# Kernel optimization log

Hardware: AMD Instinct MI355X
Metric: run time of the kernel (lower is better)

The kernel has to match this reference:

```python
import jax, jax.numpy as jnp
import numpy as np

B, S, D = 4, 2048, 512
BETA = 1.0
PARAM_SCALE = 1.0 / np.sqrt(D)  # ~ torch Linear default init scale


def setup_inputs() -> dict:
    key = jax.random.key(0)
    ks = jax.random.split(key, 14)
    def rn(k, shape, scale=1.0):
        return (jax.random.normal(k, shape, jnp.float32) * scale).astype(jnp.float32)
    return {
        "x_re": rn(ks[0], (B, S, D)),
        "x_im": rn(ks[1], (B, S, D)),
        "Wq_re": rn(ks[2], (D, D), PARAM_SCALE), "Wq_im": rn(ks[3], (D, D), PARAM_SCALE),
        "bq_re": rn(ks[4], (D,), PARAM_SCALE),   "bq_im": rn(ks[5], (D,), PARAM_SCALE),
        "Wk_re": rn(ks[6], (D, D), PARAM_SCALE), "Wk_im": rn(ks[7], (D, D), PARAM_SCALE),
        "bk_re": rn(ks[8], (D,), PARAM_SCALE),   "bk_im": rn(ks[9], (D,), PARAM_SCALE),
        "Wv_re": rn(ks[10], (D, D), PARAM_SCALE), "Wv_im": rn(ks[11], (D, D), PARAM_SCALE),
        "bv_re": rn(ks[12], (D,), PARAM_SCALE),   "bv_im": rn(ks[13], (D,), PARAM_SCALE),
    }


def reference(x_re, x_im, Wq_re, Wq_im, bq_re, bq_im,
              Wk_re, Wk_im, bk_re, bk_im, Wv_re, Wv_im, bv_re, bv_im):
    cx = lambda re, im: (re + 1j * im).astype(jnp.complex64)
    x = cx(x_re, x_im)                          # [B,S,D] complex64
    # nn.Linear: y = x @ W.T + b (complex)
    Q = jnp.einsum('bsd,ed->bse', x, cx(Wq_re, Wq_im)) + cx(bq_re, bq_im)
    K = jnp.einsum('bsd,ed->bse', x, cx(Wk_re, Wk_im)) + cx(bk_re, bk_im)
    V = jnp.einsum('bsd,ed->bse', x, cx(Wv_re, Wv_im)) + cx(bv_re, bv_im)
    # energy = -Re(Q K^H); attn = softmax(-beta * energy) = softmax(beta * Re(Q K^H))
    scores = jnp.real(jnp.einsum('bse,bte->bst', Q, jnp.conj(K)))  # [B,S,S] float32
    attn = jax.nn.softmax(BETA * scores, axis=-1)
    out = jnp.einsum('bst,bte->bse', attn.astype(jnp.complex64), V)  # [B,S,D] complex64
    return out
```

## Files before the change

kernel.cpp:

```cpp
#include <hip/hip_runtime.h>
#include <hip/hip_bf16.h>
#include <cstdint>
#include <cstddef>


typedef unsigned short u16;
typedef __attribute__((ext_vector_type(8))) _Float16 half8;
typedef __attribute__((ext_vector_type(4))) float f32x4;

#define B_    4
#define S_    2048
#define D_    512
#define M_TOT (B_ * S_)
#define KC    (2 * D_)
#define N1    (6 * D_)
#define LP    32
#define RE_PLANE 4194304

#define X_ELEMS  ((size_t)M_TOT * KC)
#define W_ELEMS  ((size_t)N1 * KC)
#define QK_ELEMS ((size_t)M_TOT * KC)
#define VT_ELEMS ((size_t)B_ * KC * S_)
#define AT_ELEMS ((size_t)M_TOT * S_)

__device__ __forceinline__ u16 f2h(float f) {
    _Float16 h = (_Float16)f;
    return __builtin_bit_cast(u16, h);
}
__device__ __forceinline__ float h2f(u16 b) {
    return (float)__builtin_bit_cast(_Float16, b);
}

__device__ __forceinline__ f32x4 mfma16(half8 a, half8 b, f32x4 c) {
    return __builtin_amdgcn_mfma_f32_16x16x32_f16(a, b, c, 0, 0, 0);
}

__device__ __forceinline__ void dma16(const u16* g, u16* l) {
    __builtin_amdgcn_global_load_lds(
        (const __attribute__((address_space(1))) unsigned int*)g,
        (__attribute__((address_space(3))) unsigned int*)l,
        16, 0, 0);
}

__device__ __forceinline__ void stage_dma(const u16* __restrict__ src, int ld,
                                          int rowbase, int kbase,
                                          u16* __restrict__ dst, int tid) {
#pragma unroll
    for (int i = 0; i < 2; ++i) {
        int c = tid + 256 * i;
        int row = c >> 2, q = c & 3;
        dma16(src + (size_t)(rowbase + row) * ld + kbase + q * 8, dst + c * 8);
    }
}

__device__ __forceinline__ void stage_half(u16* __restrict__ plane,
                                           const u16* __restrict__ src,
                                           int rowbase, int kcol, int tid) {
#pragma unroll
    for (int i = 0; i < 2; ++i) {
        int c = tid + (i << 9);
        int c2 = c ^ (((c >> 5) & 1) << 1);
        int row = ((c2 >> 3) << 1) | ((c2 >> 2) & 1);
        int ks = c2 & 3;
        dma16(src + (size_t)(rowbase + row) * KC + (kcol + ks * 8),
              plane + c * 8);
    }
}

#define VMW(N) asm volatile("s_waitcnt vmcnt(" #N ")" ::: "memory")

__global__ void k_diag(float* __restrict__ out, int out_size, float val) {
    int i = blockIdx.x * 256 + threadIdx.x;
    if (i < out_size && i < 4096) out[i] = val;
}

__global__ void k_prep(const float* __restrict__ xr, const float* __restrict__ xi,
                       const float* __restrict__ Wqr, const float* __restrict__ Wqi,
                       const float* __restrict__ Wkr, const float* __restrict__ Wki,
                       const float* __restrict__ Wvr, const float* __restrict__ Wvi,
                       const float* __restrict__ bqr, const float* __restrict__ bqi,
                       const float* __restrict__ bkr, const float* __restrict__ bki,
                       const float* __restrict__ bvr, const float* __restrict__ bvi,
                       u16* __restrict__ Xh, u16* __restrict__ Xl,
                       u16* __restrict__ Wh, float* __restrict__ bc) {
    int gb = blockIdx.x;
    int tid = threadIdx.x;
    if (gb < 16384) {
        int id = gb * 256 + tid;
        int m = id >> 9, d = id & 511;
        size_t o = (size_t)m * KC + d;
        if (o + D_ >= X_ELEMS) return;
        float vr = xr[id], vi = xi[id];
        u16 h;
        h = f2h(vr); Xh[o] = h;        Xl[o] = f2h(vr - h2f(h));
        h = f2h(vi); Xh[o + D_] = h;   Xl[o + D_] = f2h(vi - h2f(h));
    } else if (gb < 16384 + 12288) {
        int id = (gb - 16384) * 256 + tid;
        int n = id >> 10, k = id & 1023;
        int q = n >> 9, e = n & 511;
        int half = k >> 9, d = k & 511;
        const float* Wre = (q < 2) ? Wqr : ((q < 4) ? Wkr : Wvr);
        const float* Wim = (q < 2) ? Wqi : ((q < 4) ? Wki : Wvi);
        size_t src = (size_t)e * D_ + d;
        float v;
        if ((q & 1) == 0) v = half ? -Wim[src] : Wre[src];
        else              v = half ?  Wre[src] : Wim[src];
        if ((size_t)id < W_ELEMS) Wh[id] = f2h(v);
    } else {
        int id = (gb - 16384 - 12288) * 256 + tid;
        if (id >= N1) return;
        int q = id >> 9, e = id & 511;
        const float* src = (q == 0) ? bqr : (q == 1) ? bqi : (q == 2) ? bkr
                         : (q == 3) ? bki : (q == 4) ? bvr : bvi;
        bc[id] = src[e];
    }
}

#define GTILE(P, STG0, STG1, W1, STG2, STG3, W3)                              \
  {                                                                           \
    const int p_ = (P);                                                       \
    _Pragma("unroll")                                                         \
    for (int q = 0; q < 4; ++q) {                                             \
      const int kh = q >> 1, mg = q & 1;                                      \
      const u16* pa = &lds[(p_ << 2) | kh][0];                                \
      const u16* pb = &lds[(p_ << 2) | 2 | kh][0];                            \
      half8 a[4];                                                             \
      if (mg == 0) {                                                          \
        _Pragma("unroll")                                                     \
        for (int j = 0; j < 4; ++j)                                           \
          b[j] = *(const half8*)(pb + boffs + j * 512);                       \
      }                                                                       \
      _Pragma("unroll")                                                       \
      for (int i = 0; i < 4; ++i)                                             \
        a[i] = *(const half8*)(pa + aoffs + (mg * 4 + i) * 512);              \
      if (q == 0)      { STG0; }                                              \
      else if (q == 1) { STG1; W1; }                                          \
      else if (q == 2) { STG2; }                                              \
      else             { STG3; W3; }                                          \
      __builtin_amdgcn_s_barrier();                                           \
      __builtin_amdgcn_s_setprio(1);                                          \
      _Pragma("unroll")                                                       \
      for (int j = 0; j < 4; ++j) {                                           \
        _Pragma("unroll")                                                     \
        for (int i = 0; i < 4; ++i)                                           \
          acc[mg * 4 + i][j] = mfma16(a[i], b[j], acc[mg * 4 + i][j]);        \
      }                                                                       \
      __builtin_amdgcn_s_setprio(0);                                          \
      __builtin_amdgcn_s_barrier();                                           \
    }                                                                         \
  }

__global__ __launch_bounds__(512, 2) void k_gemm1(
    const u16* __restrict__ Xh, const u16* __restrict__ Xl,
    const u16* __restrict__ Wh,
    const float* __restrict__ bc,
    u16* __restrict__ Qh, u16* __restrict__ Ql,
    u16* __restrict__ Kh, u16* __restrict__ Kl,
    u16* __restrict__ VT) {
    __shared__ __attribute__((aligned(16))) u16 lds[8][8192];
    int tid = threadIdx.x;

    int orig = blockIdx.y * 12 + blockIdx.x;
    int swz = (orig & 7) * 48 + (orig >> 3);
    int bx = swz % 12, by = swz / 12;
    int nb = bx * 256, mb = by * 256;
    int g = bx >> 2;
    bool vblk = (g == 2);
    int NT = vblk ? 16 : 32;

    int lane = tid & 63, wave = tid >> 6;
    int wm = (wave >> 2) * 128, wn = (wave & 3) * 64;
    int lr = lane & 15, lq = lane >> 4;
    int lqs8 = (lq ^ (((lr >> 3) & 1) << 1)) * 8;
    int aoffs = (wm + lr) * 32 + lqs8;
    int boffs = (wn + lr) * 32 + lqs8;

    f32x4 acc[8][4] = {};
    half8 b[4];

    stage_half(&lds[0][0], Xh, mb, 0, tid);
    stage_half(&lds[2][0], Wh, nb, 0, tid);
    stage_half(&lds[1][0], Xh, mb, 32, tid);
    stage_half(&lds[3][0], Wh, nb, 32, tid);
    stage_half(&lds[4][0], Xh, mb, 64, tid);
    stage_half(&lds[6][0], Wh, nb, 64, tid);
    VMW(8);
    __builtin_amdgcn_s_barrier();

    for (int t = 0; t < NT - 2; ++t) {
        const int p = t & 1;
        const u16* s1 = (!vblk && (t + 1) >= 16) ? Xl : Xh;
        const int k1o = (((t + 1) & 15) << 6) + 32;
        const u16* s2 = (!vblk && (t + 2) >= 16) ? Xl : Xh;
        const int k2o = ((t + 2) & 15) << 6;
        GTILE(p,
              stage_half(&lds[((p ^ 1) << 2) | 1][0], s1, mb, k1o, tid),
              stage_half(&lds[((p ^ 1) << 2) | 3][0], Wh, nb, k1o, tid),
              VMW(8),
              stage_half(&lds[(p << 2) | 0][0], s2, mb, k2o, tid),
              stage_half(&lds[(p << 2) | 2][0], Wh, nb, k2o, tid),
              VMW(8));
    }
    {
        const int p = (NT - 2) & 1;
        const u16* s1 = vblk ? Xh : Xl;
        const int k1o = (((NT - 1) & 15) << 6) + 32;
        GTILE(p,
              stage_half(&lds[((p ^ 1) << 2) | 1][0], s1, mb, k1o, tid),
              stage_half(&lds[((p ^ 1) << 2) | 3][0], Wh, nb, k1o, tid),
              VMW(8),
              (void)0, (void)0,
              VMW(4));
    }
    {
        const int p = (NT - 1) & 1;
        GTILE(p, (void)0, (void)0, VMW(0), (void)0, (void)0, (void)0);
    }

#pragma unroll
    for (int j = 0; j < 4; ++j) {
        int n_g = nb + wn + j * 16 + lr;
        float bias = bc[n_g];
        int c = n_g & 1023;
#pragma unroll
        for (int i = 0; i < 8; ++i) {
            int m0 = mb + wm + i * 16 + lq * 4;
            if (vblk) {
                int bidx = m0 >> 11, s0 = m0 & 2047;
                u16 pk[4];
#pragma unroll
                for (int r = 0; r < 4; ++r) pk[r] = f2h(acc[i][j][r] + bias);
                size_t idx = ((size_t)(bidx * KC + c)) * S_ + s0;
                if (idx + 3 < VT_ELEMS)
                    *(ushort4*)&VT[idx] = make_ushort4(pk[0], pk[1], pk[2], pk[3]);
            } else {
                u16* dh = g ? Kh : Qh;
                u16* dl = g ? Kl : Ql;
#pragma unroll
                for (int r = 0; r < 4; ++r) {
                    float v = acc[i][j][r] + bias;
                    u16 h = f2h(v);
                    size_t idx = (size_t)(m0 + r) * KC + c;
                    if (idx < QK_ELEMS) {
                        dh[idx] = h;
                        dl[idx] = f2h(v - h2f(h));
                    }
                }
            }
        }
    }
}

__global__ __launch_bounds__(256) void k_gemm2(
    const u16* __restrict__ Qh, const u16* __restrict__ Ql,
    const u16* __restrict__ Kh, const u16* __restrict__ Kl,
    float* __restrict__ SC, int zbase) {
    __shared__ __attribute__((aligned(16))) u16 sAh[128 * LP], sAl[128 * LP],
                                                sBh[128 * LP], sBl[128 * LP];
    int tid = threadIdx.x;
    int nb = blockIdx.x * 128, mb = blockIdx.y * 128;
    int z = zbase + blockIdx.z;
    const u16* Ah = Qh + (size_t)z * S_ * KC;
    const u16* Al = Ql + (size_t)z * S_ * KC;
    const u16* Bh = Kh + (size_t)z * S_ * KC;
    const u16* Bl = Kl + (size_t)z * S_ * KC;
    int lane = tid & 63, wave = tid >> 6;
    int wm = (wave >> 1) * 64, wn = (wave & 1) * 64;
    int lr = lane & 15, lq = lane >> 4;
    f32x4 acc[4][4] = {};

    for (int k0 = 0; k0 < KC; k0 += 32) {
        __syncthreads();
        stage_dma(Ah, KC, mb, k0, sAh, tid);
        stage_dma(Al, KC, mb, k0, sAl, tid);
        stage_dma(Bh, KC, nb, k0, sBh, tid);
        stage_dma(Bl, KC, nb, k0, sBl, tid);
        __syncthreads();
        half8 ah[4], al[4], bh[4], bl[4];
#pragma unroll
        for (int i = 0; i < 4; ++i) {
            int ra = wm + i * 16 + lr;
            ah[i] = *(const half8*)&sAh[ra * LP + lq * 8];
            al[i] = *(const half8*)&sAl[ra * LP + lq * 8];
            int rb = wn + i * 16 + lr;
            bh[i] = *(const half8*)&sBh[rb * LP + lq * 8];
            bl[i] = *(const half8*)&sBl[rb * LP + lq * 8];
        }
#pragma unroll
        for (int i = 0; i < 4; ++i)
#pragma unroll
            for (int j = 0; j < 4; ++j) {
                acc[i][j] = mfma16(ah[i], bh[j], acc[i][j]);
                acc[i][j] = mfma16(al[i], bh[j], acc[i][j]);
                acc[i][j] = mfma16(ah[i], bl[j], acc[i][j]);
            }
    }

    size_t sc_limit = (size_t)gridDim.z * S_ * S_;
#pragma unroll
    for (int j = 0; j < 4; ++j) {
        int t = nb + wn + j * 16 + lr;
#pragma unroll
        for (int i = 0; i < 4; ++i) {
            int s0 = mb + wm + i * 16 + lq * 4;
#pragma unroll
            for (int r = 0; r < 4; ++r) {
                size_t idx = ((size_t)blockIdx.z * S_ + s0 + r) * S_ + t;
                if (idx < sc_limit) SC[idx] = acc[i][j][r];
            }
        }
    }
}

__global__ __launch_bounds__(256) void k_softmax(const float* __restrict__ SC,
                                                 u16* __restrict__ AT, int zbase) {
    int row = blockIdx.x;
    const float* src = SC + (size_t)row * S_;
    size_t drow = (size_t)zbase * S_ + row;
    u16* dst = AT + drow * S_;
    int tid = threadIdx.x;
    float v[8];
#pragma unroll
    for (int i = 0; i < 8; ++i) v[i] = src[tid + i * 256];
    float m = v[0];
#pragma unroll
    for (int i = 1; i < 8; ++i) m = fmaxf(m, v[i]);
    for (int off = 32; off > 0; off >>= 1) m = fmaxf(m, __shfl_down(m, off));
    __shared__ float redm[4], reds[4];
    if ((tid & 63) == 0) redm[tid >> 6] = m;
    __syncthreads();
    m = fmaxf(fmaxf(redm[0], redm[1]), fmaxf(redm[2], redm[3]));
    float s = 0.f;
#pragma unroll
    for (int i = 0; i < 8; ++i) { v[i] = __expf(v[i] - m); s += v[i]; }
    for (int off = 32; off > 0; off >>= 1) s += __shfl_down(s, off);
    if ((tid & 63) == 0) reds[tid >> 6] = s;
    __syncthreads();
    float inv = 1.0f / (reds[0] + reds[1] + reds[2] + reds[3]);
    if (drow * S_ + 2047 < AT_ELEMS) {
#pragma unroll
        for (int i = 0; i < 8; ++i) dst[tid + i * 256] = f2h(v[i] * inv);
    }
}

__global__ __launch_bounds__(256) void k_gemm3(
    const u16* __restrict__ AT, const u16* __restrict__ VT,
    float* __restrict__ out, int out_size, int full) {
    __shared__ __attribute__((aligned(16))) u16 sA[128 * LP], sB[128 * LP];
    int tid = threadIdx.x;
    int nb = blockIdx.x * 128, mb = blockIdx.y * 128, z = blockIdx.z;
    const u16* Abase = AT + (size_t)z * S_ * S_;
    const u16* Bbase = VT + (size_t)z * KC * S_;
    int lane = tid & 63, wave = tid >> 6;
    int wm = (wave >> 1) * 64, wn = (wave & 1) * 64;
    int lr = lane & 15, lq = lane >> 4;
    f32x4 acc[4][4] = {};

    for (int k0 = 0; k0 < S_; k0 += 32) {
        __syncthreads();
        stage_dma(Abase, S_, mb, k0, sA, tid);
        stage_dma(Bbase, S_, nb, k0, sB, tid);
        __syncthreads();
        half8 a[4], b[4];
#pragma unroll
        for (int i = 0; i < 4; ++i) {
            a[i] = *(const half8*)&sA[(wm + i * 16 + lr) * LP + lq * 8];
            b[i] = *(const half8*)&sB[(wn + i * 16 + lr) * LP + lq * 8];
        }
#pragma unroll
        for (int i = 0; i < 4; ++i)
#pragma unroll
            for (int j = 0; j < 4; ++j)
                acc[i][j] = mfma16(a[i], b[j], acc[i][j]);
    }

#pragma unroll
    for (int j = 0; j < 4; ++j) {
        int f = nb + wn + j * 16 + lr;
#pragma unroll
        for (int i = 0; i < 4; ++i) {
            int s0 = mb + wm + i * 16 + lq * 4;
#pragma unroll
            for (int r = 0; r < 4; ++r) {
                size_t base = ((size_t)z * S_ + s0 + r) * D_;
                if (f < D_) {
                    size_t o = base + f;
                    if (o < (size_t)out_size) out[o] = acc[i][j][r];
                } else if (full) {
                    size_t o = (size_t)RE_PLANE + base + (f - D_);
                    if (o < (size_t)out_size) out[o] = acc[i][j][r];
                }
            }
        }
    }
}


extern "C" void kernel_launch(void* const* d_in, const int* in_sizes, int n_in,
                              void* d_out, int out_size, void* d_ws, size_t ws_size,
                              hipStream_t stream) {
    (void)in_sizes; (void)n_in;
    const float* xr  = (const float*)d_in[0];
    const float* xi  = (const float*)d_in[1];
    const float* Wqr = (const float*)d_in[2];
    const float* Wqi = (const float*)d_in[3];
    const float* bqr = (const float*)d_in[4];
    const float* bqi = (const float*)d_in[5];
    const float* Wkr = (const float*)d_in[6];
    const float* Wki = (const float*)d_in[7];
    const float* bkr = (const float*)d_in[8];
    const float* bki = (const float*)d_in[9];
    const float* Wvr = (const float*)d_in[10];
    const float* Wvi = (const float*)d_in[11];
    const float* bvr = (const float*)d_in[12];
    const float* bvi = (const float*)d_in[13];
    float* out = (float*)d_out;

    constexpr size_t SZ_X  = X_ELEMS * 2;
    constexpr size_t SZ_W  = W_ELEMS * 2;
    constexpr size_t SZ_BC = (size_t)N1 * 4;
    constexpr size_t SZ_QK = QK_ELEMS * 2;
    constexpr size_t SZ_VT = VT_ELEMS * 2;
    constexpr size_t SZ_SC_B = (size_t)S_ * S_ * 4;

    char* p = (char*)d_ws;
    size_t off = 0;
    auto take = [&](size_t sz) {
        char* r = p + off;
        off += (sz + 255) & ~(size_t)255;
        return r;
    };
    u16*   Xh = (u16*)take(SZ_X);
    u16*   Xl = (u16*)take(SZ_X);
    u16*   Wh = (u16*)take(SZ_W);
    float* bc = (float*)take(SZ_BC);
    u16*   Qh = (u16*)take(SZ_QK);
    u16*   Ql = (u16*)take(SZ_QK);
    u16*   Kh = (u16*)take(SZ_QK);
    u16*   Kl = (u16*)take(SZ_QK);
    u16*   VT = (u16*)take(SZ_VT);
    u16*   AT = Xh;
    float* SC = (float*)(p + off);

    int nz = 0;
    if (ws_size > off) nz = (int)((ws_size - off) / SZ_SC_B);
    if (nz > B_) nz = B_;
    if (nz < 1) {
        k_diag<<<16, 256, 0, stream>>>(out, out_size, 1000.0f + (float)(ws_size >> 20));
        return;
    }

    int full = (out_size >= 2 * RE_PLANE) ? 1 : 0;

    k_prep<<<16384 + 12288 + 12, 256, 0, stream>>>(
        xr, xi, Wqr, Wqi, Wkr, Wki, Wvr, Wvi,
        bqr, bqi, bkr, bki, bvr, bvi, Xh, Xl, Wh, bc);
    k_gemm1<<<dim3(N1 / 256, M_TOT / 256), 512, 0, stream>>>(Xh, Xl, Wh, bc, Qh, Ql, Kh, Kl, VT);

    for (int z0 = 0; z0 < B_; z0 += nz) {
        int zc = (B_ - z0 < nz) ? (B_ - z0) : nz;
        k_gemm2<<<dim3(S_ / 128, S_ / 128, zc), 256, 0, stream>>>(Qh, Ql, Kh, Kl, SC, z0);
        k_softmax<<<zc * S_, 256, 0, stream>>>(SC, AT, z0);
    }
    k_gemm3<<<dim3(KC / 128, S_ / 128, B_), 256, 0, stream>>>(AT, VT, out, out_size, full);
}
```

Before: 437.0 us.

## Software-pipeline LDS fragment reads against MFMA in gemm1 and reorder block schedule

After: 412.2 us. 1.06x faster.

```diff
diff --git a/kernel.cpp b/kernel.cpp
--- a/kernel.cpp
+++ b/kernel.cpp
@@ -68,6 +68,7 @@
 }
 
 #define VMW(N) asm volatile("s_waitcnt vmcnt(" #N ")" ::: "memory")
+#define BAR()  __builtin_amdgcn_s_barrier()
 
 __global__ void k_diag(float* __restrict__ out, int out_size, float val) {
     int i = blockIdx.x * 256 + threadIdx.x;
@@ -116,39 +117,34 @@
     }
 }
 
-#define GTILE(P, STG0, STG1, W1, STG2, STG3, W3)                              \
-  {                                                                           \
-    const int p_ = (P);                                                       \
+
+#define RDA(d, pl, mg)                                                        \
+  { const u16* _pa = &lds[pl][0];                                             \
     _Pragma("unroll")                                                         \
-    for (int q = 0; q < 4; ++q) {                                             \
-      const int kh = q >> 1, mg = q & 1;                                      \
-      const u16* pa = &lds[(p_ << 2) | kh][0];                                \
-      const u16* pb = &lds[(p_ << 2) | 2 | kh][0];                            \
-      half8 a[4];                                                             \
-      if (mg == 0) {                                                          \
-        _Pragma("unroll")                                                     \
-        for (int j = 0; j < 4; ++j)                                           \
-          b[j] = *(const half8*)(pb + boffs + j * 512);                       \
-      }                                                                       \
+    for (int _i = 0; _i < 4; ++_i)                                            \
+      d[_i] = *(const half8*)(_pa + aoffs + ((mg) * 4 + _i) * 512); }
+#define RDB(d, pl)                                                            \
+  { const u16* _pb = &lds[pl][0];                                             \
+    _Pragma("unroll")                                                         \
+    for (int _i = 0; _i < 4; ++_i)                                            \
+      d[_i] = *(const half8*)(_pb + boffs + _i * 512); }
+#define MF16(av, bv, mg)                                                      \
+  { __builtin_amdgcn_s_setprio(1);                                            \
+    _Pragma("unroll")                                                         \
+    for (int _j = 0; _j < 4; ++_j) {                                          \
       _Pragma("unroll")                                                       \
-      for (int i = 0; i < 4; ++i)                                             \
-        a[i] = *(const half8*)(pa + aoffs + (mg * 4 + i) * 512);              \
-      if (q == 0)      { STG0; }                                              \
-      else if (q == 1) { STG1; W1; }                                          \
-      else if (q == 2) { STG2; }                                              \
-      else             { STG3; W3; }                                          \
-      __builtin_amdgcn_s_barrier();                                           \
-      __builtin_amdgcn_s_setprio(1);                                          \
-      _Pragma("unroll")                                                       \
-      for (int j = 0; j < 4; ++j) {                                           \
-        _Pragma("unroll")                                                     \
-        for (int i = 0; i < 4; ++i)                                           \
-          acc[mg * 4 + i][j] = mfma16(a[i], b[j], acc[mg * 4 + i][j]);        \
-      }                                                                       \
-      __builtin_amdgcn_s_setprio(0);                                          \
-      __builtin_amdgcn_s_barrier();                                           \
+      for (int _i = 0; _i < 4; ++_i)                                          \
+        acc[(mg) * 4 + _i][_j] =                                              \
+            mfma16(av[_i], bv[_j], acc[(mg) * 4 + _i][_j]);                   \
     }                                                                         \
-  }
+    __builtin_amdgcn_s_setprio(0); }
+
+#define W0(P, STG, WT) { MF16(aA, bA, 0); RDA(aB, ((P) << 2) | 0, 1); STG; WT; BAR(); }
+#define W1(P, STG)     { MF16(aB, bA, 1); RDB(bB, ((P) << 2) | 3); RDA(aA, ((P) << 2) | 1, 0); STG; BAR(); }
+#define W2(P, STG, WT) { MF16(aA, bB, 0); RDA(aB, ((P) << 2) | 1, 1); STG; WT; BAR(); }
+#define W3(P, STG)     { MF16(aB, bB, 1); RDB(bA, (((P) ^ 1) << 2) | 2); RDA(aA, (((P) ^ 1) << 2) | 0, 0); STG; BAR(); }
+#define W3L()          { MF16(aB, bB, 1); }
+#define NOP_ ((void)0)
 
 __global__ __launch_bounds__(512, 2) void k_gemm1(
     const u16* __restrict__ Xh, const u16* __restrict__ Xl,
@@ -160,9 +156,16 @@
     __shared__ __attribute__((aligned(16))) u16 lds[8][8192];
     int tid = threadIdx.x;
 
-    int orig = blockIdx.y * 12 + blockIdx.x;
-    int swz = (orig & 7) * 48 + (orig >> 3);
-    int bx = swz % 12, by = swz / 12;
+    int L = blockIdx.y * 12 + blockIdx.x;
+    int bx, by;
+    if (L < 256) {
+        int q = (L & 7) * 32 + (L >> 3);
+        bx = q & 7; by = q >> 3;
+    } else {
+        int v = L - 256;
+        int vv = (v & 7) * 16 + (v >> 3);
+        bx = 8 + (vv & 3); by = vv >> 2;
+    }
     int nb = bx * 256, mb = by * 256;
     int g = bx >> 2;
     bool vblk = (g == 2);
@@ -176,7 +179,7 @@
     int boffs = (wn + lr) * 32 + lqs8;
 
     f32x4 acc[8][4] = {};
-    half8 b[4];
+    half8 aA[4], aB[4], bA[4], bB[4];
 
     stage_half(&lds[0][0], Xh, mb, 0, tid);
     stage_half(&lds[2][0], Wh, nb, 0, tid);
@@ -185,36 +188,34 @@
     stage_half(&lds[4][0], Xh, mb, 64, tid);
     stage_half(&lds[6][0], Wh, nb, 64, tid);
     VMW(8);
-    __builtin_amdgcn_s_barrier();
+    BAR();
+    RDB(bA, 2);
+    RDA(aA, 0, 0);
 
     for (int t = 0; t < NT - 2; ++t) {
         const int p = t & 1;
         const u16* s1 = (!vblk && (t + 1) >= 16) ? Xl : Xh;
-        const int k1o = (((t + 1) & 15) << 6) + 32;
+        const int k1 = (((t + 1) & 15) << 6) + 32;
         const u16* s2 = (!vblk && (t + 2) >= 16) ? Xl : Xh;
-        const int k2o = ((t + 2) & 15) << 6;
-        GTILE(p,
-              stage_half(&lds[((p ^ 1) << 2) | 1][0], s1, mb, k1o, tid),
-              stage_half(&lds[((p ^ 1) << 2) | 3][0], Wh, nb, k1o, tid),
-              VMW(8),
-              stage_half(&lds[(p << 2) | 0][0], s2, mb, k2o, tid),
-              stage_half(&lds[(p << 2) | 2][0], Wh, nb, k2o, tid),
-              VMW(8));
+        const int k2 = ((t + 2) & 15) << 6;
+        W0(p, stage_half(&lds[((p ^ 1) << 2) | 1][0], s1, mb, k1, tid), VMW(6));
+        W1(p, stage_half(&lds[((p ^ 1) << 2) | 3][0], Wh, nb, k1, tid));
+        W2(p, stage_half(&lds[(p << 2) | 0][0], s2, mb, k2, tid), VMW(6));
+        W3(p, stage_half(&lds[(p << 2) | 2][0], Wh, nb, k2, tid));
     }
     {
-        const int p = (NT - 2) & 1;
         const u16* s1 = vblk ? Xh : Xl;
-        const int k1o = (((NT - 1) & 15) << 6) + 32;
-        GTILE(p,
-              stage_half(&lds[((p ^ 1) << 2) | 1][0], s1, mb, k1o, tid),
-              stage_half(&lds[((p ^ 1) << 2) | 3][0], Wh, nb, k1o, tid),
-              VMW(8),
-              (void)0, (void)0,
-              VMW(4));
+        const int k1 = (((NT - 1) & 15) << 6) + 32;
+        W0(0, stage_half(&lds[(1 << 2) | 1][0], s1, mb, k1, tid), VMW(6));
+        W1(0, stage_half(&lds[(1 << 2) | 3][0], Wh, nb, k1, tid));
+        W2(0, NOP_, VMW(4));
+        W3(0, NOP_);
     }
     {
-        const int p = (NT - 1) & 1;
-        GTILE(p, (void)0, (void)0, VMW(0), (void)0, (void)0, (void)0);
+        W0(1, NOP_, VMW(0));
+        W1(1, NOP_);
+        W2(1, NOP_, NOP_);
+        W3L();
     }
 
 #pragma unroll
@@ -455,7 +456,7 @@
     k_prep<<<16384 + 12288 + 12, 256, 0, stream>>>(
         xr, xi, Wqr, Wqi, Wkr, Wki, Wvr, Wvi,
         bqr, bqi, bkr, bki, bvr, bvi, Xh, Xl, Wh, bc);
-    k_gemm1<<<dim3(N1 / 256, M_TOT / 256), 512, 0, stream>>>(Xh, Xl, Wh, bc, Qh, Ql, Kh, Kl, VT);
+    k_gemm1<<<dim3(12, 32), 512, 0, stream>>>(Xh, Xl, Wh, bc, Qh, Ql, Kh, Kl, VT);
 
     for (int z0 = 0; z0 < B_; z0 += nz) {
         int zc = (B_ - z0 < nz) ? (B_ - z0) : nz;
```
